# Kernel optimization log

Hardware: AMD Instinct MI355X
Metric: run time of the kernel (lower is better)

Reference implementation:

```python
import jax, jax.numpy as jnp
import numpy as np

SUBNET_NUM = 32
BATCH = 131072
H1, H2 = 10, 6          # subnet_arch = [10, 6]
SMOOTH_LAMBDA = 0.001
BN_EPS = 1e-10


def setup_inputs() -> dict:
    key = jax.random.key(0)
    ks = jax.random.split(key, 7)
    f32 = jnp.float32
    x = jax.random.normal(ks[0], (BATCH, SUBNET_NUM), f32)
    # small init scale keeps tanh in its non-saturated (smooth) regime
    W1 = 0.5 * jax.random.normal(ks[1], (SUBNET_NUM, 1, H1), f32)
    b1 = 0.1 * jax.random.normal(ks[2], (SUBNET_NUM, H1), f32)
    W2 = 0.5 * jax.random.normal(ks[3], (SUBNET_NUM, H1, H2), f32)
    b2 = 0.1 * jax.random.normal(ks[4], (SUBNET_NUM, H2), f32)
    W3 = 0.5 * jax.random.normal(ks[5], (SUBNET_NUM, H2, 1), f32)
    b3 = 0.1 * jax.random.normal(ks[6], (SUBNET_NUM, 1), f32)
    return {"x": x, "W1": W1, "b1": b1, "W2": W2, "b2": b2, "W3": W3, "b3": b3}


def _subnet_scalar(x_s, w1, b1, w2, b2, w3, b3):
    """One subnet applied to one scalar input: output and d2out/dx2."""
    def f(xs):
        h = jnp.tanh(xs * w1[0] + b1)        # [H1]  (input dim is 1)
        h = jnp.tanh(h @ w2 + b2)            # [H2]
        return (h @ w3)[0] + b3[0]           # scalar
    out = f(x_s)
    g2 = jax.grad(jax.grad(f))(x_s)          # second derivative wrt the scalar input
    return out, g2


def reference(x, W1, b1, W2, b2, W3, b3):
    # vmap over batch (inner) and over subnets (outer, axis 1 of x / axis 0 of params)
    per_batch = jax.vmap(_subnet_scalar, in_axes=(0, None, None, None, None, None, None))
    per_subnet = jax.vmap(per_batch, in_axes=(1, 0, 0, 0, 0, 0, 0), out_axes=(1, 1))
    out, g2 = per_subnet(x, W1, b1, W2, b2, W3, b3)      # each [BATCH, SUBNET_NUM]

    # BatchNorm (momentum=0.0, center=False, scale=False) in training mode:
    # normalize by batch stats; moving_variance == biased batch variance.
    mean = jnp.mean(out, axis=0)
    var = jnp.mean((out - mean) ** 2, axis=0)
    out_bn = (out - mean) * jax.lax.rsqrt(var + BN_EPS)

    # smooth penalty per subnet: mean(grad2^2) / sqrt(moving_variance)
    penalty = jnp.mean(g2 ** 2, axis=0) / jnp.sqrt(var)
    smooth_loss = SMOOTH_LAMBDA * jnp.sum(penalty)
    return out_bn, smooth_loss
```

## Files before the change

kernel.cpp:

```cpp
#include <hip/hip_runtime.h>

#define BATCH 131072
#define SN 32
#define H1 10
#define H2 6
#define ROWS 128
#define GRID (BATCH / ROWS)
#define TPB 512
#define LDS_STRIDE 33

typedef float v2f __attribute__((ext_vector_type(2)));

__device__ __forceinline__ v2f bc(float s) { v2f r; r.x = s; r.y = s; return r; }
__device__ __forceinline__ v2f fma2(v2f a, v2f b, v2f c) {
    return __builtin_elementwise_fma(a, b, c);
}
__device__ __forceinline__ v2f tanh2(v2f x) {
    v2f x2 = x + x;
    v2f e; e.x = __expf(x2.x); e.y = __expf(x2.y);
    v2f e1 = e + bc(1.0f);
    v2f r; r.x = __builtin_amdgcn_rcpf(e1.x); r.y = __builtin_amdgcn_rcpf(e1.y);
    return fma2(bc(-2.0f), r, bc(1.0f));
}

__device__ __forceinline__ float wave_sum(float v) {
    v += __int_as_float(__builtin_amdgcn_update_dpp(
            0, __float_as_int(v), 0x111, 0xf, 0xf, false));
    v += __int_as_float(__builtin_amdgcn_update_dpp(
            0, __float_as_int(v), 0x112, 0xf, 0xf, false));
    v += __int_as_float(__builtin_amdgcn_update_dpp(
            0, __float_as_int(v), 0x114, 0xf, 0xf, false));
    v += __int_as_float(__builtin_amdgcn_update_dpp(
            0, __float_as_int(v), 0x118, 0xf, 0xf, false));
    v += __int_as_float(__builtin_amdgcn_update_dpp(
            0, __float_as_int(v), 0x142, 0xa, 0xf, false));
    v += __int_as_float(__builtin_amdgcn_update_dpp(
            0, __float_as_int(v), 0x143, 0xc, 0xf, false));
    return v;
}

__global__ __launch_bounds__(TPB) void k_main(
    const float* __restrict__ x,
    const float* __restrict__ W1, const float* __restrict__ B1,
    const float* __restrict__ W2, const float* __restrict__ B2,
    const float* __restrict__ W3, const float* __restrict__ B3,
    float* __restrict__ out, float* __restrict__ partial )
{
    __shared__ float xt[ROWS * LDS_STRIDE];
    const int tid = threadIdx.x;
    const int lane = tid & 63;
    const int wave = tid >> 6;
    const int blk = blockIdx.x;

    const float4* xv = (const float4*)(x + (size_t)blk * ROWS * SN);
    #pragma unroll
    for (int it = 0; it < 2; ++it) {
        int v = it * TPB + tid;
        float4 val = xv[v];
        int r = v >> 3;
        int c = (v & 7) << 2;
        float* dst = &xt[r * LDS_STRIDE + c];
        dst[0] = val.x; dst[1] = val.y; dst[2] = val.z; dst[3] = val.w;
    }
    __syncthreads();

    #pragma unroll 1
    for (int si = 0; si < 4; ++si) {
        const int s = __builtin_amdgcn_readfirstlane(si * 8 + wave);
        const float* w1p = W1 + s * H1;
        const float* b1p = B1 + s * H1;
        const float* w2p = W2 + s * H1 * H2;
        const float* b2p = B2 + s * H2;
        const float* w3p = W3 + s * H2;
        const float b3 = B3[s];

        float w1r[H1], b1r[H1];
        #pragma unroll
        for (int i = 0; i < H1; ++i) { w1r[i] = w1p[i]; b1r[i] = b1p[i]; }
        float w2r[H1 * H2];
        #pragma unroll
        for (int k = 0; k < H1 * H2; ++k) w2r[k] = w2p[k];
        float b2r[H2], w3r[H2];
        #pragma unroll
        for (int j = 0; j < H2; ++j) { b2r[j] = b2p[j]; w3r[j] = w3p[j]; }

        v2f xs;
        xs.x = xt[lane * LDS_STRIDE + s];
        xs.y = xt[(lane + 64) * LDS_STRIDE + s];

        v2f t[H1], p[H1], q[H1];
        #pragma unroll
        for (int i = 0; i < H1; ++i) {
            v2f u = fma2(xs, bc(w1r[i]), bc(b1r[i]));
            v2f ti = tanh2(u);
            v2f e = fma2(-ti, ti, bc(1.0f));
            t[i] = ti;
            p[i] = e * bc(w1r[i]);
            q[i] = (ti * p[i]) * bc(w1r[i]);
        }

        v2f o = bc(b3), g2a = bc(0.0f);
        #pragma unroll
        for (int j = 0; j < H2; ++j) {
            v2f vv = bc(b2r[j]), a = bc(0.0f), c = bc(0.0f);
            #pragma unroll
            for (int i = 0; i < H1; ++i) {
                v2f wb = bc(w2r[i * H2 + j]);
                vv = fma2(wb, t[i], vv);
                a  = fma2(wb, p[i], a);
                c  = fma2(wb, q[i], c);
            }
            v2f sj = tanh2(vv);
            v2f dj = fma2(-sj, sj, bc(1.0f));
            v2f aa = a * a;
            v2f h  = fma2(sj, aa, c);
            v2f k  = dj * h;
            o   = fma2(bc(w3r[j]), sj, o);
            g2a = fma2(bc(w3r[j]), k, g2a);
        }

        xt[lane * LDS_STRIDE + s] = o.x;
        xt[(lane + 64) * LDS_STRIDE + s] = o.y;

        v2f s2v = o * o;
        v2f s3v = (g2a * g2a) * bc(4.0f);
        float s1 = wave_sum(o.x + o.y);
        float s2 = wave_sum(s2v.x + s2v.y);
        float s3 = wave_sum(s3v.x + s3v.y);
        if (lane == 63) {
            partial[(size_t)(0 * SN + s) * GRID + blk] = s1;
            partial[(size_t)(1 * SN + s) * GRID + blk] = s2;
            partial[(size_t)(2 * SN + s) * GRID + blk] = s3;
        }
    }
    __syncthreads();

    float4* po = (float4*)out;
    const size_t base = (size_t)blk * (ROWS * SN / 4);
    #pragma unroll
    for (int it = 0; it < 2; ++it) {
        int v = it * TPB + tid;
        int r = v >> 3;
        int c = (v & 7) << 2;
        const float* src = &xt[r * LDS_STRIDE + c];
        float4 w; w.x = src[0]; w.y = src[1]; w.z = src[2]; w.w = src[3];
        po[base + v] = w;
    }
}

__global__ __launch_bounds__(256) void k_reduce(const float* __restrict__ partial,
                                                double* __restrict__ acc)
{
    const float* p = partial + (size_t)blockIdx.x * GRID;
    double s = 0.0;
    for (int i = threadIdx.x; i < GRID; i += 256) s += (double)p[i];
    #pragma unroll
    for (int off = 32; off > 0; off >>= 1) s += __shfl_down(s, off);
    __shared__ double ws[4];
    if ((threadIdx.x & 63) == 0) ws[threadIdx.x >> 6] = s;
    __syncthreads();
    if (threadIdx.x == 0) acc[blockIdx.x] = ws[0] + ws[1] + ws[2] + ws[3];
}

__global__ __launch_bounds__(256) void k_norm(float* __restrict__ out,
                                              const double* __restrict__ acc)
{
    __shared__ float mean_s[SN], inv_s[SN];
    const int tid = threadIdx.x;
    if (tid < SN) {
        const double invB = 1.0 / (double)BATCH;
        double mean = acc[tid] * invB;
        double var = acc[SN + tid] * invB - mean * mean;
        if (var < 0.0) var = 0.0;
        mean_s[tid] = (float)mean;
        inv_s[tid] = (float)(1.0 / sqrt(var + 1e-10));
    }
    if (blockIdx.x == 0 && tid == 0) {
        const double invB = 1.0 / (double)BATCH;
        double sum = 0.0;
        for (int s = 0; s < SN; ++s) {
            double mean = acc[s] * invB;
            double var = acc[SN + s] * invB - mean * mean;
            if (var < 0.0) var = 0.0;
            sum += (acc[2 * SN + s] * invB) / sqrt(var);
        }
        out[(size_t)BATCH * SN] = (float)(0.001 * sum);
    }
    __syncthreads();
    const int v = blockIdx.x * 256 + tid;
    float4* p = (float4*)out;
    float4 val = p[v];
    const int c = (v & 7) << 2;
    val.x = (val.x - mean_s[c + 0]) * inv_s[c + 0];
    val.y = (val.y - mean_s[c + 1]) * inv_s[c + 1];
    val.z = (val.z - mean_s[c + 2]) * inv_s[c + 2];
    val.w = (val.w - mean_s[c + 3]) * inv_s[c + 3];
    p[v] = val;
}

extern "C" void kernel_launch(void* const* d_in, const int* in_sizes, int n_in,
                              void* d_out, int out_size, void* d_ws, size_t ws_size,
                              hipStream_t stream) {
    const float* x  = (const float*)d_in[0];
    const float* W1 = (const float*)d_in[1];
    const float* B1 = (const float*)d_in[2];
    const float* W2 = (const float*)d_in[3];
    const float* B2 = (const float*)d_in[4];
    const float* W3 = (const float*)d_in[5];
    const float* B3 = (const float*)d_in[6];

    float* out = (float*)d_out;
    float* partial = (float*)d_ws;
    double* acc = (double*)((char*)d_ws + (size_t)3 * SN * GRID * sizeof(float));

    k_main<<<GRID, TPB, 0, stream>>>(x, W1, B1, W2, B2, W3, B3, out, partial);
    k_reduce<<<3 * SN, 256, 0, stream>>>(partial, acc);
    k_norm<<<(BATCH * SN / 4) / 256, 256, 0, stream>>>(out, acc);
}
```

Before: 120.8 us.

## Fuse partial-sum reduction into normalization kernel with grid-stride loop

Merges the separate reduce and normalize kernels into one finish kernel. Each of 512 blocks redundantly reduces all 96 partial rows of 1024 floats into shared doubles, then normalizes the output with a grid-stride loop instead of one float4 per thread. This removes one kernel launch and the global acc round trip. In exchange, every block repeats the reduction, adding redundant reads of the partial buffer.

```diff
diff --git a/kernel.cpp b/kernel.cpp
--- a/kernel.cpp
+++ b/kernel.cpp
@@ -8,6 +8,9 @@
 #define GRID (BATCH / ROWS)
 #define TPB 512
 #define LDS_STRIDE 33
+
+#define FB 512
+#define FT 256
 
 typedef float v2f __attribute__((ext_vector_type(2)));
 
@@ -148,54 +151,60 @@
     }
 }
 
-__global__ __launch_bounds__(256) void k_reduce(const float* __restrict__ partial,
-                                                double* __restrict__ acc)
+__global__ __launch_bounds__(FT) void k_finish(float* __restrict__ out,
+                                               const float* __restrict__ partial)
 {
-    const float* p = partial + (size_t)blockIdx.x * GRID;
-    double s = 0.0;
-    for (int i = threadIdx.x; i < GRID; i += 256) s += (double)p[i];
-    #pragma unroll
-    for (int off = 32; off > 0; off >>= 1) s += __shfl_down(s, off);
-    __shared__ double ws[4];
-    if ((threadIdx.x & 63) == 0) ws[threadIdx.x >> 6] = s;
-    __syncthreads();
-    if (threadIdx.x == 0) acc[blockIdx.x] = ws[0] + ws[1] + ws[2] + ws[3];
-}
-
-__global__ __launch_bounds__(256) void k_norm(float* __restrict__ out,
-                                              const double* __restrict__ acc)
-{
+    __shared__ double red_s[3 * SN];
     __shared__ float mean_s[SN], inv_s[SN];
     const int tid = threadIdx.x;
+    const int lane = tid & 63;
+    const int wave = tid >> 6;
+
+    for (int r = wave; r < 3 * SN; r += 4) {
+        const float4* pr = (const float4*)(partial + (size_t)r * GRID);
+        double sd = 0.0;
+        #pragma unroll
+        for (int k = 0; k < 4; ++k) {
+            float4 v4 = pr[k * 64 + lane];
+            sd += (double)v4.x + (double)v4.y + (double)v4.z + (double)v4.w;
+        }
+        #pragma unroll
+        for (int off = 32; off > 0; off >>= 1) sd += __shfl_down(sd, off);
+        if (lane == 0) red_s[r] = sd;
+    }
+    __syncthreads();
+
+    const double invB = 1.0 / (double)BATCH;
     if (tid < SN) {
-        const double invB = 1.0 / (double)BATCH;
-        double mean = acc[tid] * invB;
-        double var = acc[SN + tid] * invB - mean * mean;
+        double mean = red_s[tid] * invB;
+        double var = red_s[SN + tid] * invB - mean * mean;
         if (var < 0.0) var = 0.0;
         mean_s[tid] = (float)mean;
         inv_s[tid] = (float)(1.0 / sqrt(var + 1e-10));
     }
     if (blockIdx.x == 0 && tid == 0) {
-        const double invB = 1.0 / (double)BATCH;
         double sum = 0.0;
         for (int s = 0; s < SN; ++s) {
-            double mean = acc[s] * invB;
-            double var = acc[SN + s] * invB - mean * mean;
+            double mean = red_s[s] * invB;
+            double var = red_s[SN + s] * invB - mean * mean;
             if (var < 0.0) var = 0.0;
-            sum += (acc[2 * SN + s] * invB) / sqrt(var);
+            sum += (red_s[2 * SN + s] * invB) / sqrt(var);
         }
         out[(size_t)BATCH * SN] = (float)(0.001 * sum);
     }
     __syncthreads();
-    const int v = blockIdx.x * 256 + tid;
+
     float4* p = (float4*)out;
-    float4 val = p[v];
-    const int c = (v & 7) << 2;
-    val.x = (val.x - mean_s[c + 0]) * inv_s[c + 0];
-    val.y = (val.y - mean_s[c + 1]) * inv_s[c + 1];
-    val.z = (val.z - mean_s[c + 2]) * inv_s[c + 2];
-    val.w = (val.w - mean_s[c + 3]) * inv_s[c + 3];
-    p[v] = val;
+    const int total = BATCH * SN / 4;
+    for (int v = blockIdx.x * FT + tid; v < total; v += FB * FT) {
+        float4 val = p[v];
+        const int c = (v & 7) << 2;
+        val.x = (val.x - mean_s[c + 0]) * inv_s[c + 0];
+        val.y = (val.y - mean_s[c + 1]) * inv_s[c + 1];
+        val.z = (val.z - mean_s[c + 2]) * inv_s[c + 2];
+        val.w = (val.w - mean_s[c + 3]) * inv_s[c + 3];
+        p[v] = val;
+    }
 }
 
 extern "C" void kernel_launch(void* const* d_in, const int* in_sizes, int n_in,
@@ -211,9 +220,7 @@
 
     float* out = (float*)d_out;
     float* partial = (float*)d_ws;
-    double* acc = (double*)((char*)d_ws + (size_t)3 * SN * GRID * sizeof(float));
 
     k_main<<<GRID, TPB, 0, stream>>>(x, W1, B1, W2, B2, W3, B3, out, partial);
-    k_reduce<<<3 * SN, 256, 0, stream>>>(partial, acc);
-    k_norm<<<(BATCH * SN / 4) / 256, 256, 0, stream>>>(out, acc);
-}
+    k_finish<<<FB, FT, 0, stream>>>(out, partial);
+}
```

Result: slower. 132.2 us (+9.4%).
